# Kernel tuning notes

Measured on AMD Instinct MI355X. Metric: run time of the kernel, lower is better.

## Reference

```python
import jax, jax.numpy as jnp
import numpy as np

B, S, D = 4, 2048, 1024
H = 16
DK = D // H  # 64

def setup_inputs() -> dict:
    key = jax.random.key(0)
    ks = jax.random.split(key, 5)
    scale = 0.02
    return {
        "x": jax.random.normal(ks[0], (B, S, D), dtype=jnp.float32),
        "Wq": jax.random.normal(ks[1], (D, D), dtype=jnp.float32) * scale,
        "Wk": jax.random.normal(ks[2], (D, D), dtype=jnp.float32) * scale,
        "Wv": jax.random.normal(ks[3], (D, D), dtype=jnp.float32) * scale,
        "Wo": jax.random.normal(ks[4], (D, D), dtype=jnp.float32) * scale,
    }

def reference(x, Wq, Wk, Wv, Wo):
    b, s, d = x.shape
    h, dk = H, DK
    # torch nn.Linear(bias=False): y = x @ W.T
    q = (x @ Wq.T).reshape(b, s, h, dk).transpose(0, 2, 1, 3)  # [b,h,s,dk]
    k = (x @ Wk.T).reshape(b, s, h, dk).transpose(0, 2, 1, 3)
    v = (x @ Wv.T).reshape(b, s, h, dk).transpose(0, 2, 1, 3)
    scores = jnp.einsum('bhqd,bhkd->bhqk', q, k) * (dk ** -0.5)
    causal = jnp.triu(jnp.ones((s, s), dtype=bool), k=1)  # True = masked out
    scores = jnp.where(causal, -jnp.inf, scores)
    probs = jax.nn.softmax(scores, axis=-1)
    attn = jnp.einsum('bhqk,bhkd->bhqd', probs, v)  # [b,h,s,dk]
    attn = attn.transpose(0, 2, 1, 3).reshape(b, s, d)
    return attn @ Wo.T
```

## Files before the change

### kernel.cpp

```cpp
#include <hip/hip_runtime.h>

typedef __attribute__((ext_vector_type(8))) short bf16x8;
typedef __attribute__((ext_vector_type(4))) float f32x4;
typedef unsigned int u32;
typedef unsigned short u16;

constexpr int Bb = 4, S = 2048, D = 1024, H = 16, DK = 64, M = Bb * S;

#if __has_builtin(__builtin_amdgcn_exp2f)
#define EXP2F __builtin_amdgcn_exp2f
#else
#define EXP2F exp2f
#endif

__device__ __forceinline__ u16 f2bf(float f) {
  u32 u = __float_as_uint(f);
  return (u16)((u + 0x7fffu + ((u >> 16) & 1u)) >> 16);
}

__device__ __forceinline__ void gld_lds16(const u16* g, u16* l) {
  __builtin_amdgcn_global_load_lds((const __attribute__((address_space(1))) u32*)g,
                                   (__attribute__((address_space(3))) u32*)l, 16, 0, 0);
}

__global__ void cast_kernel(const float* __restrict__ s, u16* __restrict__ d, int n) {
  int i = (blockIdx.x * blockDim.x + threadIdx.x) * 4;
  if (i >= n) return;
  float4 f = *(const float4*)(s + i);
  ushort4 o;
  o.x = f2bf(f.x); o.y = f2bf(f.y); o.z = f2bf(f.z); o.w = f2bf(f.w);
  *(ushort4*)(d + i) = o;
}

struct CastArgs { const float* s[4]; u16* d[4]; float sc[4]; };
__global__ void cast4_kernel(CastArgs a) {
  int i = (blockIdx.x * blockDim.x + threadIdx.x) * 4;
  int w = i >> 20;
  int off = i & ((1 << 20) - 1);
  float sc = a.sc[w];
  float4 f = *(const float4*)(a.s[w] + off);
  ushort4 o;
  o.x = f2bf(f.x * sc); o.y = f2bf(f.y * sc); o.z = f2bf(f.z * sc); o.w = f2bf(f.w * sc);
  *(ushort4*)(a.d[w] + off) = o;
}

template <bool OUTF32>
__device__ __forceinline__ void gemm_core(const u16* __restrict__ A,
                                          const u16* __restrict__ Bt,
                                          float* __restrict__ Cf, u16* __restrict__ Cb,
                                          int Nn, int Kk, int m0, int n0,
                                          u16* As, u16* Bs) {
  const int tid = threadIdx.x, wave = tid >> 6, lane = tid & 63;
  const int quad = lane >> 4, col = lane & 15;
  const int wm = wave >> 1, wn = wave & 1;

  f32x4 acc[4][4];
#pragma unroll
  for (int i = 0; i < 4; i++)
#pragma unroll
    for (int j = 0; j < 4; j++) acc[i][j] = (f32x4){0.f, 0.f, 0.f, 0.f};

  for (int k0 = 0; k0 < Kk; k0 += 64) {
#pragma unroll
    for (int j = 0; j < 4; j++) {
      int g = (wave * 4 + j) * 64;
      int gl = g + lane;
      int r = gl >> 3, sl = gl & 7;
      int kof = (sl ^ (r & 7)) * 8;
      const u16* ga = A + (size_t)(m0 + r) * Kk + k0 + kof;
      gld_lds16(ga, &As[g * 8]);
      const u16* gb = Bt + (size_t)(n0 + r) * Kk + k0 + kof;
      gld_lds16(gb, &Bs[g * 8]);
    }
    __syncthreads();
#pragma unroll
    for (int kb = 0; kb < 2; kb++) {
      bf16x8 af[4], bfr[4];
#pragma unroll
      for (int mi = 0; mi < 4; mi++) {
        int R = wm * 64 + mi * 16 + col;
        af[mi] = *(const bf16x8*)&As[R * 64 + (((kb * 4 + quad) ^ (R & 7)) << 3)];
      }
#pragma unroll
      for (int ni = 0; ni < 4; ni++) {
        int R = wn * 64 + ni * 16 + col;
        bfr[ni] = *(const bf16x8*)&Bs[R * 64 + (((kb * 4 + quad) ^ (R & 7)) << 3)];
      }
#pragma unroll
      for (int mi = 0; mi < 4; mi++)
#pragma unroll
        for (int ni = 0; ni < 4; ni++)
          acc[mi][ni] = __builtin_amdgcn_mfma_f32_16x16x32_bf16(af[mi], bfr[ni], acc[mi][ni], 0, 0, 0);
    }
    __syncthreads();
  }
#pragma unroll
  for (int mi = 0; mi < 4; mi++)
#pragma unroll
    for (int ni = 0; ni < 4; ni++)
#pragma unroll
      for (int r = 0; r < 4; r++) {
        int row = m0 + wm * 64 + mi * 16 + quad * 4 + r;
        int cc = n0 + wn * 64 + ni * 16 + col;
        float v = acc[mi][ni][r];
        if (OUTF32) Cf[(size_t)row * Nn + cc] = v;
        else Cb[(size_t)row * Nn + cc] = f2bf(v);
      }
}

struct QkvArgs { const u16* bt[3]; u16* c[3]; };
__global__ __launch_bounds__(256) void gemm_qkv(const u16* __restrict__ A, QkvArgs q) {
  __shared__ __align__(16) u16 As[128 * 64];
  __shared__ __align__(16) u16 Bs[128 * 64];
  int sel = blockIdx.x >> 3;
  int n0 = (blockIdx.x & 7) * 128, m0 = blockIdx.y * 128;
  gemm_core<false>(A, q.bt[sel], nullptr, q.c[sel], D, D, m0, n0, As, Bs);
}

__global__ __launch_bounds__(256) void gemm_f32(const u16* __restrict__ A,
                                                const u16* __restrict__ Bt,
                                                float* __restrict__ C) {
  __shared__ __align__(16) u16 As[128 * 64];
  __shared__ __align__(16) u16 Bs[128 * 64];
  gemm_core<true>(A, Bt, C, nullptr, D, D, blockIdx.y * 128, blockIdx.x * 128, As, Bs);
}

__global__ __launch_bounds__(256) void attn_kernel(const u16* __restrict__ Q,
                                                   const u16* __restrict__ K,
                                                   const u16* __restrict__ V,
                                                   u16* __restrict__ O) {
  __shared__ __align__(16) u16 Vt[2][64 * 64];
  __shared__ __align__(16) u16 Pw[4][32 * 64];
  const int tid = threadIdx.x, wave = tid >> 6, lane = tid & 63;
  const int quad = lane >> 4, col = lane & 15;
  const int bh = blockIdx.x, b = bh >> 4, h = bh & 15;
  const int ya = blockIdx.y & 3, yk = blockIdx.y >> 2;
  const int qb = (yk == 0) ? ya : (yk == 1) ? 7 - ya : (yk == 2) ? 8 + ya : 15 - ya;
  const size_t base = (size_t)b * S * D + h * DK;
  const int qw = qb * 128 + wave * 32;

  bf16x8 aq[2][2];
#pragma unroll
  for (int mi = 0; mi < 2; mi++)
#pragma unroll
    for (int kb = 0; kb < 2; kb++)
      aq[mi][kb] = *(const bf16x8*)(Q + base + (size_t)(qw + mi * 16 + col) * D + kb * 32 + quad * 8);

  f32x4 ao[2][4], lacc[2];
#pragma unroll
  for (int mi = 0; mi < 2; mi++) {
    lacc[mi] = (f32x4){0.f, 0.f, 0.f, 0.f};
#pragma unroll
    for (int dg = 0; dg < 4; dg++) ao[mi][dg] = (f32x4){0.f, 0.f, 0.f, 0.f};
  }
  bf16x8 bones;
#pragma unroll
  for (int e = 0; e < 8; e++) bones[e] = (short)0x3F80;

  const int vkey = tid >> 2;
  const int vdof = (tid & 3) * 16;
  const int nkt = 2 * qb + 2;

  bf16x8 vA0, vA1, vB0, vB1;
  {
    const u16* vp = V + base + (size_t)vkey * D + vdof;
    vA0 = *(const bf16x8*)vp; vA1 = *(const bf16x8*)(vp + 8);
  }
  {
    const u16* vp = V + base + (size_t)(64 + vkey) * D + vdof;
    vB0 = *(const bf16x8*)vp; vB1 = *(const bf16x8*)(vp + 8);
  }

  auto vstage = [&](int buf, bf16x8 v0, bf16x8 v1) {
#pragma unroll
    for (int g = 0; g < 2; g++) {
      int dof = vdof + g * 8;
      int sw = (((vkey >> 3) ^ (dof >> 3)) & 7) * 8 + (vkey & 7);
      bf16x8 vv = g ? v1 : v0;
#pragma unroll
      for (int e = 0; e < 8; e++) Vt[buf][(dof + e) * 64 + sw] = (u16)vv[e];
    }
  };
  vstage(0, vA0, vA1);

  auto body = [&](int kt, bool ph) {
    __syncthreads();
    const int bf = ph ? 1 : 0, nb = bf ^ 1;
    const bool active = (kt * 64 <= qw + 31);
    bf16x8 bk0[4], bk1[4];
    if (active) {
#pragma unroll
      for (int n16 = 0; n16 < 4; n16++) {
        const u16* kp = K + base + (size_t)(kt * 64 + n16 * 16 + col) * D + quad * 8;
        bk0[n16] = *(const bf16x8*)kp;
        bk1[n16] = *(const bf16x8*)(kp + 32);
      }
    }
    if (kt + 1 < nkt) {
      vstage(nb, ph ? vA0 : vB0, ph ? vA1 : vB1);
      if (kt + 2 < nkt) {
        const u16* vp = V + base + (size_t)((kt + 2) * 64 + vkey) * D + vdof;
        if (ph) { vB0 = *(const bf16x8*)vp; vB1 = *(const bf16x8*)(vp + 8); }
        else    { vA0 = *(const bf16x8*)vp; vA1 = *(const bf16x8*)(vp + 8); }
      }
    }
    if (!active) return;
    f32x4 sacc[2][4];
#pragma unroll
    for (int mi = 0; mi < 2; mi++)
#pragma unroll
      for (int n16 = 0; n16 < 4; n16++) sacc[mi][n16] = (f32x4){0.f, 0.f, 0.f, 0.f};
#pragma unroll
    for (int mi = 0; mi < 2; mi++)
#pragma unroll
      for (int n16 = 0; n16 < 4; n16++) {
        sacc[mi][n16] = __builtin_amdgcn_mfma_f32_16x16x32_bf16(aq[mi][0], bk0[n16], sacc[mi][n16], 0, 0, 0);
        sacc[mi][n16] = __builtin_amdgcn_mfma_f32_16x16x32_bf16(aq[mi][1], bk1[n16], sacc[mi][n16], 0, 0, 0);
      }
    const bool full = (kt * 64 + 63) <= qw;
#pragma unroll
    for (int mi = 0; mi < 2; mi++)
#pragma unroll
      for (int r = 0; r < 4; r++) {
        int qloc = mi * 16 + quad * 4 + r;
        int qs = quad << 1;
#pragma unroll
        for (int n16 = 0; n16 < 4; n16++) {
          float p = EXP2F(sacc[mi][n16][r]);
          if (!full) {
            int kg = kt * 64 + n16 * 16 + col;
            p = (kg > qw + qloc) ? 0.f : p;
          }
          int kgl = n16 * 16 + col;
          int perm = ((kgl >> 3) ^ qs) & 7;
          Pw[wave][qloc * 64 + perm * 8 + (kgl & 7)] = (u16)(__float_as_uint(p) >> 16);
        }
      }
    bf16x8 bv[2][4];
#pragma unroll
    for (int kb = 0; kb < 2; kb++)
#pragma unroll
      for (int dg = 0; dg < 4; dg++) {
        int d3 = (dg * 2 + (col >> 3)) & 7;
        bv[kb][dg] = *(const bf16x8*)&Vt[bf][(dg * 16 + col) * 64 + (((kb * 4 + quad) ^ d3) << 3)];
      }
#pragma unroll
    for (int mi = 0; mi < 2; mi++) {
      int qs2 = ((col >> 2) & 3) << 1;
      bf16x8 ap0 = *(const bf16x8*)&Pw[wave][(mi * 16 + col) * 64 + (((quad ^ qs2) & 7) << 3)];
      bf16x8 ap1 = *(const bf16x8*)&Pw[wave][(mi * 16 + col) * 64 + ((((4 + quad) ^ qs2) & 7) << 3)];
#pragma unroll
      for (int dg = 0; dg < 4; dg++) {
        ao[mi][dg] = __builtin_amdgcn_mfma_f32_16x16x32_bf16(ap0, bv[0][dg], ao[mi][dg], 0, 0, 0);
        ao[mi][dg] = __builtin_amdgcn_mfma_f32_16x16x32_bf16(ap1, bv[1][dg], ao[mi][dg], 0, 0, 0);
      }
      lacc[mi] = __builtin_amdgcn_mfma_f32_16x16x32_bf16(ap0, bones, lacc[mi], 0, 0, 0);
      lacc[mi] = __builtin_amdgcn_mfma_f32_16x16x32_bf16(ap1, bones, lacc[mi], 0, 0, 0);
    }
  };

  for (int kt = 0; kt < nkt; kt += 2) {
    body(kt, false);
    body(kt + 1, true);
  }

#pragma unroll
  for (int mi = 0; mi < 2; mi++)
#pragma unroll
    for (int r = 0; r < 4; r++) {
      float inv = 1.f / lacc[mi][r];
      int q = qw + mi * 16 + quad * 4 + r;
#pragma unroll
      for (int dg = 0; dg < 4; dg++)
        O[base + (size_t)q * D + dg * 16 + col] = f2bf(ao[mi][dg][r] * inv);
    }
}

extern "C" void kernel_launch(void* const* d_in, const int* in_sizes, int n_in,
                              void* d_out, int out_size, void* d_ws, size_t ws_size,
                              hipStream_t stream) {
  const float* x  = (const float*)d_in[0];
  const float* Wq = (const float*)d_in[1];
  const float* Wk = (const float*)d_in[2];
  const float* Wv = (const float*)d_in[3];
  const float* Wo = (const float*)d_in[4];

  u16* xb  = (u16*)d_ws;
  u16* wqb = xb + (size_t)M * D;
  u16* wkb = wqb + (size_t)D * D;
  u16* wvb = wkb + (size_t)D * D;
  u16* wob = wvb + (size_t)D * D;
  u16* Qb  = wob + (size_t)D * D;
  u16* Kb  = Qb + (size_t)M * D;
  u16* Vb  = Kb + (size_t)M * D;
  u16* Ab  = xb;

  cast_kernel<<<M * D / 1024, 256, 0, stream>>>(x, xb, M * D);
  CastArgs ca;
  ca.s[0] = Wq; ca.s[1] = Wk; ca.s[2] = Wv; ca.s[3] = Wo;
  ca.d[0] = wqb; ca.d[1] = wkb; ca.d[2] = wvb; ca.d[3] = wob;
  ca.sc[0] = 0.18033688011112042f;
  ca.sc[1] = 1.f; ca.sc[2] = 1.f; ca.sc[3] = 1.f;
  cast4_kernel<<<4 * D * D / 1024, 256, 0, stream>>>(ca);

  QkvArgs qa;
  qa.bt[0] = wqb; qa.bt[1] = wkb; qa.bt[2] = wvb;
  qa.c[0] = Qb; qa.c[1] = Kb; qa.c[2] = Vb;
  gemm_qkv<<<dim3(24, M / 128), 256, 0, stream>>>(xb, qa);

  attn_kernel<<<dim3(Bb * H, S / 128), 256, 0, stream>>>(Qb, Kb, Vb, Ab);

  gemm_f32<<<dim3(D / 128, M / 128), 256, 0, stream>>>(Ab, wob, (float*)d_out);
}
```

Before: 298.3 us.

## Pair causal query blocks per workgroup and stage K tiles in LDS via async loads

After: 266.4 us. -10.7%, faster.

```diff
diff --git a/kernel.cpp b/kernel.cpp
--- a/kernel.cpp
+++ b/kernel.cpp
@@ -129,151 +129,158 @@
                                                    const u16* __restrict__ K,
                                                    const u16* __restrict__ V,
                                                    u16* __restrict__ O) {
+  __shared__ __align__(16) u16 Ks[2][2][64 * 32];
   __shared__ __align__(16) u16 Vt[2][64 * 64];
   __shared__ __align__(16) u16 Pw[4][32 * 64];
   const int tid = threadIdx.x, wave = tid >> 6, lane = tid & 63;
   const int quad = lane >> 4, col = lane & 15;
   const int bh = blockIdx.x, b = bh >> 4, h = bh & 15;
-  const int ya = blockIdx.y & 3, yk = blockIdx.y >> 2;
-  const int qb = (yk == 0) ? ya : (yk == 1) ? 7 - ya : (yk == 2) ? 8 + ya : 15 - ya;
+  const int pair = blockIdx.y;
   const size_t base = (size_t)b * S * D + h * DK;
-  const int qw = qb * 128 + wave * 32;
-
-  bf16x8 aq[2][2];
-#pragma unroll
-  for (int mi = 0; mi < 2; mi++)
-#pragma unroll
-    for (int kb = 0; kb < 2; kb++)
-      aq[mi][kb] = *(const bf16x8*)(Q + base + (size_t)(qw + mi * 16 + col) * D + kb * 32 + quad * 8);
-
-  f32x4 ao[2][4], lacc[2];
-#pragma unroll
-  for (int mi = 0; mi < 2; mi++) {
-    lacc[mi] = (f32x4){0.f, 0.f, 0.f, 0.f};
-#pragma unroll
-    for (int dg = 0; dg < 4; dg++) ao[mi][dg] = (f32x4){0.f, 0.f, 0.f, 0.f};
+
+  const int vk0 = (tid & 31) * 2;
+  const int vdg = tid >> 5;
+
+  bf16x8 bones;
+#pragma unroll
+  for (int e = 0; e < 8; e++) bones[e] = (short)0x3F80;
+
+  for (int half = 0; half < 2; half++) {
+    const int qb = half ? pair : 15 - pair;
+    const int qw = qb * 128 + wave * 32;
+    const int nkt = 2 * qb + 2;
+
+    bf16x8 aq[2][2];
+#pragma unroll
+    for (int mi = 0; mi < 2; mi++)
+#pragma unroll
+      for (int kb = 0; kb < 2; kb++)
+        aq[mi][kb] = *(const bf16x8*)(Q + base + (size_t)(qw + mi * 16 + col) * D + kb * 32 + quad * 8);
+
+    f32x4 ao[2][4], lacc[2];
+#pragma unroll
+    for (int mi = 0; mi < 2; mi++) {
+      lacc[mi] = (f32x4){0.f, 0.f, 0.f, 0.f};
+#pragma unroll
+      for (int dg = 0; dg < 4; dg++) ao[mi][dg] = (f32x4){0.f, 0.f, 0.f, 0.f};
+    }
+
+    bf16x8 vA0, vA1, vB0, vB1;
+    {
+      const u16* vp = V + base + (size_t)vk0 * D + vdg * 8;
+      vA0 = *(const bf16x8*)vp; vA1 = *(const bf16x8*)(vp + D);
+    }
+    __syncthreads();
+    {
+      int c = tid, cb = wave * 64;
+      const u16* g0 = K + base + (size_t)(c >> 2) * D + (c & 3) * 8;
+      gld_lds16(g0, &Ks[0][0][cb * 8]);
+      gld_lds16(g0 + 32, &Ks[0][1][cb * 8]);
+    }
+    auto vstage = [&](int buf, bf16x8 r0, bf16x8 r1) {
+      int kgrp = vk0 >> 3, kin = vk0 & 7;
+      int perm = (kgrp ^ vdg) & 7;
+#pragma unroll
+      for (int e = 0; e < 8; e++) {
+        u32 val = ((u32)(u16)r0[e]) | ((u32)(u16)r1[e] << 16);
+        *(u32*)&Vt[buf][(vdg * 8 + e) * 64 + perm * 8 + kin] = val;
+      }
+    };
+    vstage(0, vA0, vA1);
+    {
+      const u16* vp = V + base + (size_t)(64 + vk0) * D + vdg * 8;
+      vB0 = *(const bf16x8*)vp; vB1 = *(const bf16x8*)(vp + D);
+    }
+
+    for (int kt = 0; kt < nkt; kt++) {
+      const int bf = kt & 1, nb = bf ^ 1, ph = kt & 1;
+      __syncthreads();
+      const bool active = (kt * 64 <= qw + 31);
+      if (kt + 1 < nkt) {
+        {
+          int c = tid, cb = wave * 64;
+          const u16* g0 = K + base + (size_t)((kt + 1) * 64 + (c >> 2)) * D + (c & 3) * 8;
+          gld_lds16(g0, &Ks[nb][0][cb * 8]);
+          gld_lds16(g0 + 32, &Ks[nb][1][cb * 8]);
+        }
+        vstage(nb, ph ? vA0 : vB0, ph ? vA1 : vB1);
+        if (kt + 2 < nkt) {
+          const u16* vp = V + base + (size_t)((kt + 2) * 64 + vk0) * D + vdg * 8;
+          if (ph) { vB0 = *(const bf16x8*)vp; vB1 = *(const bf16x8*)(vp + D); }
+          else    { vA0 = *(const bf16x8*)vp; vA1 = *(const bf16x8*)(vp + D); }
+        }
+      }
+      if (!active) continue;
+      bf16x8 bk0[4], bk1[4];
+#pragma unroll
+      for (int n16 = 0; n16 < 4; n16++) {
+        bk0[n16] = *(const bf16x8*)&Ks[bf][0][(n16 * 16 + col) * 32 + quad * 8];
+        bk1[n16] = *(const bf16x8*)&Ks[bf][1][(n16 * 16 + col) * 32 + quad * 8];
+      }
+      f32x4 sacc[2][4];
+#pragma unroll
+      for (int mi = 0; mi < 2; mi++)
+#pragma unroll
+        for (int n16 = 0; n16 < 4; n16++) sacc[mi][n16] = (f32x4){0.f, 0.f, 0.f, 0.f};
+#pragma unroll
+      for (int mi = 0; mi < 2; mi++)
+#pragma unroll
+        for (int n16 = 0; n16 < 4; n16++) {
+          sacc[mi][n16] = __builtin_amdgcn_mfma_f32_16x16x32_bf16(aq[mi][0], bk0[n16], sacc[mi][n16], 0, 0, 0);
+          sacc[mi][n16] = __builtin_amdgcn_mfma_f32_16x16x32_bf16(aq[mi][1], bk1[n16], sacc[mi][n16], 0, 0, 0);
+        }
+      const bool full = (kt * 64 + 63) <= qw;
+#pragma unroll
+      for (int mi = 0; mi < 2; mi++)
+#pragma unroll
+        for (int r = 0; r < 4; r++) {
+          int qloc = mi * 16 + quad * 4 + r;
+          int qs = quad << 1;
+#pragma unroll
+          for (int n16 = 0; n16 < 4; n16++) {
+            float p = EXP2F(sacc[mi][n16][r]);
+            if (!full) {
+              int kg = kt * 64 + n16 * 16 + col;
+              p = (kg > qw + qloc) ? 0.f : p;
+            }
+            int kgl = n16 * 16 + col;
+            int perm = ((kgl >> 3) ^ qs) & 7;
+            Pw[wave][qloc * 64 + perm * 8 + (kgl & 7)] = (u16)(__float_as_uint(p) >> 16);
+          }
+        }
+      bf16x8 bv[2][4];
+#pragma unroll
+      for (int kb = 0; kb < 2; kb++)
+#pragma unroll
+        for (int dg = 0; dg < 4; dg++) {
+          int d3 = (dg * 2 + (col >> 3)) & 7;
+          bv[kb][dg] = *(const bf16x8*)&Vt[bf][(dg * 16 + col) * 64 + (((kb * 4 + quad) ^ d3) << 3)];
+        }
+#pragma unroll
+      for (int mi = 0; mi < 2; mi++) {
+        int qs2 = ((col >> 2) & 3) << 1;
+        bf16x8 ap0 = *(const bf16x8*)&Pw[wave][(mi * 16 + col) * 64 + (((quad ^ qs2) & 7) << 3)];
+        bf16x8 ap1 = *(const bf16x8*)&Pw[wave][(mi * 16 + col) * 64 + ((((4 + quad) ^ qs2) & 7) << 3)];
+#pragma unroll
+        for (int dg = 0; dg < 4; dg++) {
+          ao[mi][dg] = __builtin_amdgcn_mfma_f32_16x16x32_bf16(ap0, bv[0][dg], ao[mi][dg], 0, 0, 0);
+          ao[mi][dg] = __builtin_amdgcn_mfma_f32_16x16x32_bf16(ap1, bv[1][dg], ao[mi][dg], 0, 0, 0);
+        }
+        lacc[mi] = __builtin_amdgcn_mfma_f32_16x16x32_bf16(ap0, bones, lacc[mi], 0, 0, 0);
+        lacc[mi] = __builtin_amdgcn_mfma_f32_16x16x32_bf16(ap1, bones, lacc[mi], 0, 0, 0);
+      }
+    }
+#pragma unroll
+    for (int mi = 0; mi < 2; mi++)
+#pragma unroll
+      for (int r = 0; r < 4; r++) {
+        float inv = 1.f / lacc[mi][r];
+        int q = qw + mi * 16 + quad * 4 + r;
+#pragma unroll
+        for (int dg = 0; dg < 4; dg++)
+          O[base + (size_t)q * D + dg * 16 + col] = f2bf(ao[mi][dg][r] * inv);
+      }
   }
-  bf16x8 bones;
-#pragma unroll
-  for (int e = 0; e < 8; e++) bones[e] = (short)0x3F80;
-
-  const int vkey = tid >> 2;
-  const int vdof = (tid & 3) * 16;
-  const int nkt = 2 * qb + 2;
-
-  bf16x8 vA0, vA1, vB0, vB1;
-  {
-    const u16* vp = V + base + (size_t)vkey * D + vdof;
-    vA0 = *(const bf16x8*)vp; vA1 = *(const bf16x8*)(vp + 8);
-  }
-  {
-    const u16* vp = V + base + (size_t)(64 + vkey) * D + vdof;
-    vB0 = *(const bf16x8*)vp; vB1 = *(const bf16x8*)(vp + 8);
-  }
-
-  auto vstage = [&](int buf, bf16x8 v0, bf16x8 v1) {
-#pragma unroll
-    for (int g = 0; g < 2; g++) {
-      int dof = vdof + g * 8;
-      int sw = (((vkey >> 3) ^ (dof >> 3)) & 7) * 8 + (vkey & 7);
-      bf16x8 vv = g ? v1 : v0;
-#pragma unroll
-      for (int e = 0; e < 8; e++) Vt[buf][(dof + e) * 64 + sw] = (u16)vv[e];
-    }
-  };
-  vstage(0, vA0, vA1);
-
-  auto body = [&](int kt, bool ph) {
-    __syncthreads();
-    const int bf = ph ? 1 : 0, nb = bf ^ 1;
-    const bool active = (kt * 64 <= qw + 31);
-    bf16x8 bk0[4], bk1[4];
-    if (active) {
-#pragma unroll
-      for (int n16 = 0; n16 < 4; n16++) {
-        const u16* kp = K + base + (size_t)(kt * 64 + n16 * 16 + col) * D + quad * 8;
-        bk0[n16] = *(const bf16x8*)kp;
-        bk1[n16] = *(const bf16x8*)(kp + 32);
-      }
-    }
-    if (kt + 1 < nkt) {
-      vstage(nb, ph ? vA0 : vB0, ph ? vA1 : vB1);
-      if (kt + 2 < nkt) {
-        const u16* vp = V + base + (size_t)((kt + 2) * 64 + vkey) * D + vdof;
-        if (ph) { vB0 = *(const bf16x8*)vp; vB1 = *(const bf16x8*)(vp + 8); }
-        else    { vA0 = *(const bf16x8*)vp; vA1 = *(const bf16x8*)(vp + 8); }
-      }
-    }
-    if (!active) return;
-    f32x4 sacc[2][4];
-#pragma unroll
-    for (int mi = 0; mi < 2; mi++)
-#pragma unroll
-      for (int n16 = 0; n16 < 4; n16++) sacc[mi][n16] = (f32x4){0.f, 0.f, 0.f, 0.f};
-#pragma unroll
-    for (int mi = 0; mi < 2; mi++)
-#pragma unroll
-      for (int n16 = 0; n16 < 4; n16++) {
-        sacc[mi][n16] = __builtin_amdgcn_mfma_f32_16x16x32_bf16(aq[mi][0], bk0[n16], sacc[mi][n16], 0, 0, 0);
-        sacc[mi][n16] = __builtin_amdgcn_mfma_f32_16x16x32_bf16(aq[mi][1], bk1[n16], sacc[mi][n16], 0, 0, 0);
-      }
-    const bool full = (kt * 64 + 63) <= qw;
-#pragma unroll
-    for (int mi = 0; mi < 2; mi++)
-#pragma unroll
-      for (int r = 0; r < 4; r++) {
-        int qloc = mi * 16 + quad * 4 + r;
-        int qs = quad << 1;
-#pragma unroll
-        for (int n16 = 0; n16 < 4; n16++) {
-          float p = EXP2F(sacc[mi][n16][r]);
-          if (!full) {
-            int kg = kt * 64 + n16 * 16 + col;
-            p = (kg > qw + qloc) ? 0.f : p;
-          }
-          int kgl = n16 * 16 + col;
-          int perm = ((kgl >> 3) ^ qs) & 7;
-          Pw[wave][qloc * 64 + perm * 8 + (kgl & 7)] = (u16)(__float_as_uint(p) >> 16);
-        }
-      }
-    bf16x8 bv[2][4];
-#pragma unroll
-    for (int kb = 0; kb < 2; kb++)
-#pragma unroll
-      for (int dg = 0; dg < 4; dg++) {
-        int d3 = (dg * 2 + (col >> 3)) & 7;
-        bv[kb][dg] = *(const bf16x8*)&Vt[bf][(dg * 16 + col) * 64 + (((kb * 4 + quad) ^ d3) << 3)];
-      }
-#pragma unroll
-    for (int mi = 0; mi < 2; mi++) {
-      int qs2 = ((col >> 2) & 3) << 1;
-      bf16x8 ap0 = *(const bf16x8*)&Pw[wave][(mi * 16 + col) * 64 + (((quad ^ qs2) & 7) << 3)];
-      bf16x8 ap1 = *(const bf16x8*)&Pw[wave][(mi * 16 + col) * 64 + ((((4 + quad) ^ qs2) & 7) << 3)];
-#pragma unroll
-      for (int dg = 0; dg < 4; dg++) {
-        ao[mi][dg] = __builtin_amdgcn_mfma_f32_16x16x32_bf16(ap0, bv[0][dg], ao[mi][dg], 0, 0, 0);
-        ao[mi][dg] = __builtin_amdgcn_mfma_f32_16x16x32_bf16(ap1, bv[1][dg], ao[mi][dg], 0, 0, 0);
-      }
-      lacc[mi] = __builtin_amdgcn_mfma_f32_16x16x32_bf16(ap0, bones, lacc[mi], 0, 0, 0);
-      lacc[mi] = __builtin_amdgcn_mfma_f32_16x16x32_bf16(ap1, bones, lacc[mi], 0, 0, 0);
-    }
-  };
-
-  for (int kt = 0; kt < nkt; kt += 2) {
-    body(kt, false);
-    body(kt + 1, true);
-  }
-
-#pragma unroll
-  for (int mi = 0; mi < 2; mi++)
-#pragma unroll
-    for (int r = 0; r < 4; r++) {
-      float inv = 1.f / lacc[mi][r];
-      int q = qw + mi * 16 + quad * 4 + r;
-#pragma unroll
-      for (int dg = 0; dg < 4; dg++)
-        O[base + (size_t)q * D + dg * 16 + col] = f2bf(ao[mi][dg][r] * inv);
-    }
 }
 
 extern "C" void kernel_launch(void* const* d_in, const int* in_sizes, int n_in,
@@ -308,7 +315,7 @@
   qa.c[0] = Qb; qa.c[1] = Kb; qa.c[2] = Vb;
   gemm_qkv<<<dim3(24, M / 128), 256, 0, stream>>>(xb, qa);
 
-  attn_kernel<<<dim3(Bb * H, S / 128), 256, 0, stream>>>(Qb, Kb, Vb, Ab);
+  attn_kernel<<<dim3(Bb * H, 8), 256, 0, stream>>>(Qb, Kb, Vb, Ab);
 
   gemm_f32<<<dim3(D / 128, M / 128), 256, 0, stream>>>(Ab, wob, (float*)d_out);
 }
```
